# Kernel tuning notes

Measured on AMD Instinct MI355X. Metric: run time of the kernel, lower is better.

Reference implementation:

```python
import jax, jax.numpy as jnp
import numpy as np

N_NODES = 100000
N_EDGES = 1600000
D = 128


def _graph_conv(x, src, dst, norm_src, norm_dst, W, b):
    # DGL GraphConv, norm='both': out = D_dst^{-1/2} A D_src^{-1/2} x W + b
    xs = x * norm_src[:, None]                 # [N, d] scale by src (out-)degree
    agg = jax.ops.segment_sum(xs[src], dst, num_segments=N_NODES)  # SpMM
    hd = agg * norm_dst[:, None]
    return hd @ W + b


def setup_inputs() -> dict:
    key = jax.random.key(0)
    ks = jax.random.split(key, 9)
    h = jax.random.normal(ks[0], (N_NODES, D), dtype=jnp.float32)
    src = jax.random.randint(ks[1], (N_EDGES,), 0, N_NODES, dtype=jnp.int64)
    dst = jax.random.randint(ks[2], (N_EDGES,), 0, N_NODES, dtype=jnp.int64)
    s = 1.0 / np.sqrt(D)
    W0 = jax.random.uniform(ks[3], (D, D), jnp.float32, -s, s)
    b0 = jnp.zeros((D,), jnp.float32)
    W1 = jax.random.uniform(ks[4], (D, D), jnp.float32, -s, s)
    b1 = jnp.zeros((D,), jnp.float32)
    W2 = jax.random.uniform(ks[5], (D, D), jnp.float32, -s, s)
    b2 = jnp.zeros((D,), jnp.float32)
    return {"h": h, "src": src, "dst": dst, "W0": W0, "b0": b0,
            "W1": W1, "b1": b1, "W2": W2, "b2": b2}


def reference(h, src, dst, W0, b0, W1, b1, W2, b2):
    ones = jnp.ones((N_EDGES,), jnp.float32)
    deg_out = jnp.maximum(jax.ops.segment_sum(ones, src, num_segments=N_NODES), 1.0)
    deg_in = jnp.maximum(jax.ops.segment_sum(ones, dst, num_segments=N_NODES), 1.0)
    norm_src = deg_out ** -0.5
    norm_dst = deg_in ** -0.5

    x = jax.nn.relu(_graph_conv(h, src, dst, norm_src, norm_dst, W0, b0))
    x = jax.nn.relu(_graph_conv(x, src, dst, norm_src, norm_dst, W1, b1))
    x = _graph_conv(x, src, dst, norm_src, norm_dst, W2, b2)
    # dgl.mean_nodes over a single graph -> [1, out_size]
    return jnp.mean(x, axis=0, keepdims=True)
```

## Files before the change

kernel.cpp:

```cpp
#include <hip/hip_runtime.h>
#include <hip/hip_fp16.h>

#define N_NODES 100000
#define N_EDGES 1600000
#define D 128
#define SCAN_NB ((N_NODES + 1023) / 1024)
#define CHK 128
#define CHUNK_E (N_EDGES / CHK)
#define HALF_N 50000
#define HALF_U (HALF_N / 4)
#define PP_STRIDE (N_NODES / 4)
#define NSH2 2
#define SH2 (N_NODES / NSH2)
#define SH2_U (SH2 / 4)

typedef _Float16 f16x4 __attribute__((ext_vector_type(4)));
typedef _Float16 f16x8 __attribute__((ext_vector_type(8)));
typedef float f32x4 __attribute__((ext_vector_type(4)));
typedef float f32x2 __attribute__((ext_vector_type(2)));

__global__ __launch_bounds__(256) void
k_zwt(const float* __restrict__ W0, const float* __restrict__ W1,
      __half* __restrict__ Wt, uint4* __restrict__ zbase) {
    if (blockIdx.x < 128) {
        int i = blockIdx.x * 256 + threadIdx.x;
        int l = i >> 14, r = i & (D * D - 1);
        int n = r >> 7, k = r & 127;
        const float* W = l ? W1 : W0;
        Wt[i] = __float2half(W[k * D + n]);
        return;
    }
    int i = (blockIdx.x - 128) * 256 + threadIdx.x;
    if (i < 2 * N_NODES / 4) zbase[i] = (uint4){0u, 0u, 0u, 0u};
}

__global__ __launch_bounds__(256) void
k_hist(const int* __restrict__ src, const int* __restrict__ dst,
       unsigned int* __restrict__ pp, int* __restrict__ cnt_src) {
    __shared__ unsigned int h[HALF_U];
    int b = blockIdx.x;
    int half = b >> 7, c = b & (CHK - 1);
    int lo = half * HALF_N;
    for (int i = threadIdx.x; i < HALF_U; i += 256) h[i] = 0;
    __syncthreads();
    int e0 = c * CHUNK_E;
    int s0 = e0 + half * (CHUNK_E / 2);
    for (int i = s0 + threadIdx.x; i < s0 + CHUNK_E / 2; i += 256)
        atomicAdd(&cnt_src[src[i]], 1);
    for (int i = e0 + threadIdx.x; i < e0 + CHUNK_E; i += 256) {
        int v = dst[i] - lo;
        if ((unsigned)v < HALF_N)
            atomicAdd(&h[v >> 2], 1u << ((v & 3) * 8));
    }
    __syncthreads();
    unsigned int* po = pp + (size_t)c * PP_STRIDE + half * HALF_U;
    for (int i = threadIdx.x; i < HALF_U; i += 256) po[i] = h[i];
}

__global__ void k_merge(unsigned int* __restrict__ pp, int* __restrict__ cnt_dst) {
    int u = blockIdx.x * blockDim.x + threadIdx.x;
    if (u >= PP_STRIDE) return;
    unsigned int* p = pp + u;
    int s0 = 0, s1 = 0, s2 = 0, s3 = 0;
#pragma unroll 8
    for (int c = 0; c < CHK; c++) {
        unsigned int v = p[(size_t)c * PP_STRIDE];
        p[(size_t)c * PP_STRIDE] =
            (unsigned)s0 | ((unsigned)s1 << 8) | ((unsigned)s2 << 16) | ((unsigned)s3 << 24);
        s0 += v & 255; s1 += (v >> 8) & 255; s2 += (v >> 16) & 255; s3 += (v >> 24) & 255;
    }
    cnt_dst[4 * u + 0] = s0; cnt_dst[4 * u + 1] = s1;
    cnt_dst[4 * u + 2] = s2; cnt_dst[4 * u + 3] = s3;
}

__global__ __launch_bounds__(1024) void
k_scan1(const int* __restrict__ cnt_dst, int* __restrict__ rpD,
        int* __restrict__ bsD) {
    __shared__ int s[1024];
    int tid = threadIdx.x;
    int i = blockIdx.x * 1024 + tid;
    int v = (i < N_NODES) ? cnt_dst[i] : 0;
    s[tid] = v;
    __syncthreads();
    for (int d = 1; d < 1024; d <<= 1) {
        int t = (tid >= d) ? s[tid - d] : 0;
        __syncthreads();
        s[tid] += t;
        __syncthreads();
    }
    if (i < N_NODES) rpD[1 + i] = s[tid];
    if (tid == 1023) bsD[blockIdx.x] = s[1023];
}

__global__ void k_scan2(int* __restrict__ bs) {
    __shared__ int s[128];
    int tid = threadIdx.x;
    int v = (tid < SCAN_NB) ? bs[tid] : 0;
    s[tid] = v;
    __syncthreads();
    for (int d = 1; d < 128; d <<= 1) {
        int t = (tid >= d) ? s[tid - d] : 0;
        __syncthreads();
        s[tid] += t;
        __syncthreads();
    }
    if (tid < SCAN_NB) bs[tid] = s[tid] - v;
}

__global__ void k_scan3norm(int* __restrict__ rpD, const int* __restrict__ bsD,
                            const int* __restrict__ cnt_src,
                            const int* __restrict__ cnt_dst,
                            float* __restrict__ ns, float* __restrict__ nd,
                            float* __restrict__ colsum) {
    int i = blockIdx.x * blockDim.x + threadIdx.x;
    if (i >= N_NODES) return;
    rpD[1 + i] += bsD[i >> 10];
    if (i == 0) rpD[0] = 0;
    if (i < 128) colsum[i] = 0.0f;
    ns[i] = rsqrtf((float)max(cnt_src[i], 1));
    nd[i] = rsqrtf((float)max(cnt_dst[i], 1));
}

__global__ __launch_bounds__(256) void
k_scatter(const int* __restrict__ src, const int* __restrict__ dst,
          const int* __restrict__ rpD, const unsigned int* __restrict__ pp,
          const float* __restrict__ nd, int* __restrict__ csr_src,
          float* __restrict__ wsum) {
    __shared__ unsigned int cur[SH2_U];
    int bb = blockIdx.x;
    int sh = bb & 1, c = bb >> 1;
    int lo = sh * SH2;
    for (int i = threadIdx.x; i < SH2_U; i += 256) cur[i] = 0;
    __syncthreads();
    int e0 = c * CHUNK_E;
    const unsigned int* pre = pp + (size_t)c * PP_STRIDE;
    for (int i = e0 + threadIdx.x; i < e0 + CHUNK_E; i += 256) {
        int dfull = dst[i];
        int sfull = src[i];
        int d = dfull - lo;
        if ((unsigned)d < SH2) {
            int sft = (d & 3) * 8;
            int rank = (atomicAdd(&cur[d >> 2], 1u << sft) >> sft) & 255;
            int p8 = (pre[dfull >> 2] >> ((dfull & 3) * 8)) & 255;
            csr_src[rpD[dfull] + p8 + rank] = sfull;
        }
        if ((i & 1) == sh)
            unsafeAtomicAdd(&wsum[sfull], nd[dfull]);
    }
}

__global__ void k_prep(const float* __restrict__ x, const float* __restrict__ ns,
                       unsigned int* __restrict__ out) {
    int i = blockIdx.x * 256 + threadIdx.x;
    if (i >= N_NODES * (D / 4)) return;
    int n = i >> 5;
    float4 v = ((const float4*)x)[i];
    float s = ns[n];
    int u = __builtin_amdgcn_cvt_pk_fp8_f32(v.x * s, v.y * s, 0, false);
    u = __builtin_amdgcn_cvt_pk_fp8_f32(v.z * s, v.w * s, u, true);
    out[i] = (unsigned int)u;
}

__global__ __launch_bounds__(256) void
k_spmm(const unsigned char* __restrict__ x8, const int* __restrict__ row_ptr,
       const int* __restrict__ csr_src, __half* __restrict__ agg) {
    int wave = (blockIdx.x * blockDim.x + threadIdx.x) >> 6;
    int lane = threadIdx.x & 63;
    int hf = lane >> 5, l32 = lane & 31;
    if (wave >= N_NODES) return;
    int beg = row_ptr[wave], end = row_ptr[wave + 1];
    float a0 = 0.f, a1 = 0.f, a2 = 0.f, a3 = 0.f;
    int j = beg;
    for (; j + 7 < end; j += 8) {
#pragma unroll
        for (int p = 0; p < 4; p++) {
            int s0 = csr_src[j + 2 * p];
            int s1 = csr_src[j + 2 * p + 1];
            int s = hf ? s1 : s0;
            unsigned int u = *(const unsigned int*)(x8 + (size_t)s * D + 4 * l32);
            f32x2 lo = __builtin_amdgcn_cvt_pk_f32_fp8(u, false);
            f32x2 hi = __builtin_amdgcn_cvt_pk_f32_fp8(u, true);
            a0 += lo[0]; a1 += lo[1]; a2 += hi[0]; a3 += hi[1];
        }
    }
    for (; j + 1 < end; j += 2) {
        int s0 = csr_src[j], s1 = csr_src[j + 1];
        int s = hf ? s1 : s0;
        unsigned int u = *(const unsigned int*)(x8 + (size_t)s * D + 4 * l32);
        f32x2 lo = __builtin_amdgcn_cvt_pk_f32_fp8(u, false);
        f32x2 hi = __builtin_amdgcn_cvt_pk_f32_fp8(u, true);
        a0 += lo[0]; a1 += lo[1]; a2 += hi[0]; a3 += hi[1];
    }
    if (j < end && hf == 0) {
        int s = csr_src[j];
        unsigned int u = *(const unsigned int*)(x8 + (size_t)s * D + 4 * l32);
        f32x2 lo = __builtin_amdgcn_cvt_pk_f32_fp8(u, false);
        f32x2 hi = __builtin_amdgcn_cvt_pk_f32_fp8(u, true);
        a0 += lo[0]; a1 += lo[1]; a2 += hi[0]; a3 += hi[1];
    }
    a0 += __shfl_xor(a0, 32, 64);
    a1 += __shfl_xor(a1, 32, 64);
    a2 += __shfl_xor(a2, 32, 64);
    a3 += __shfl_xor(a3, 32, 64);
    if (hf == 0) {
        f16x4 o;
        o[0] = (_Float16)a0; o[1] = (_Float16)a1; o[2] = (_Float16)a2; o[3] = (_Float16)a3;
        ((f16x4*)(agg + (size_t)wave * D))[l32] = o;
    }
}

__global__ __launch_bounds__(256) void
k_gemm_mfma(const __half* __restrict__ A, const __half* __restrict__ Wt,
            const float* __restrict__ b, const float* __restrict__ nd,
            const float* __restrict__ ns, unsigned char* __restrict__ out) {
    int w = threadIdx.x >> 6, lane = threadIdx.x & 63;
    int m = lane & 15, q = lane >> 4;
    int row0 = blockIdx.x * 128 + w * 32;

    f16x8 zf;
#pragma unroll
    for (int j = 0; j < 8; j++) zf[j] = (_Float16)0;
    f16x8 af[2][4];
#pragma unroll
    for (int g = 0; g < 2; g++) {
        int arow = row0 + g * 16 + m;
        const f16x8* pa = (const f16x8*)(A + (size_t)arow * D);
        bool aok = arow < N_NODES;
#pragma unroll
        for (int ks = 0; ks < 4; ks++) af[g][ks] = aok ? pa[ks * 4 + q] : zf;
    }

    const f16x8* pb = (const f16x8*)Wt;
    f32x4 acc[2][8];
#pragma unroll
    for (int g = 0; g < 2; g++)
#pragma unroll
        for (int nt = 0; nt < 8; nt++) acc[g][nt] = (f32x4){0.f, 0.f, 0.f, 0.f};

#pragma unroll
    for (int ks = 0; ks < 4; ks++) {
#pragma unroll
        for (int nt = 0; nt < 8; nt++) {
            f16x8 bf = pb[((nt * 16 + m) << 4) + (ks << 2) + q];
            acc[0][nt] = __builtin_amdgcn_mfma_f32_16x16x32_f16(af[0][ks], bf, acc[0][nt], 0, 0, 0);
            acc[1][nt] = __builtin_amdgcn_mfma_f32_16x16x32_f16(af[1][ks], bf, acc[1][nt], 0, 0, 0);
        }
    }

#pragma unroll
    for (int g = 0; g < 2; g++) {
        int er = row0 + g * 16 + q * 4;
        float sd[4], ss[4];
#pragma unroll
        for (int r = 0; r < 4; r++) {
            int n = er + r;
            bool ok = n < N_NODES;
            sd[r] = ok ? nd[n] : 0.0f;
            ss[r] = ok ? ns[n] : 0.0f;
        }
#pragma unroll
        for (int nt = 0; nt < 8; nt++) {
            int col = nt * 16 + m;
            float bc = b[col];
#pragma unroll
            for (int r = 0; r < 4; r++) {
                int n = er + r;
                if (n < N_NODES) {
                    float v = fmaxf(sd[r] * acc[g][nt][r] + bc, 0.0f) * ss[r];
                    int pk = __builtin_amdgcn_cvt_pk_fp8_f32(v, v, 0, false);
                    out[(size_t)n * D + col] = (unsigned char)(pk & 0xff);
                }
            }
        }
    }
}

__global__ __launch_bounds__(256) void
k_gemm_red(const __half* __restrict__ A, const __half* __restrict__ Wt,
           const float* __restrict__ b, const float* __restrict__ nd,
           const float* __restrict__ ns, const float* __restrict__ wsum,
           float* __restrict__ colsum) {
    __shared__ float red[128];
    int tid = threadIdx.x;
    if (tid < 128) red[tid] = 0.0f;
    __syncthreads();

    int w = tid >> 6, lane = tid & 63;
    int m = lane & 15, q = lane >> 4;
    int row0 = blockIdx.x * 128 + w * 32;

    f16x8 zf;
#pragma unroll
    for (int j = 0; j < 8; j++) zf[j] = (_Float16)0;
    f16x8 af[2][4];
#pragma unroll
    for (int g = 0; g < 2; g++) {
        int arow = row0 + g * 16 + m;
        const f16x8* pa = (const f16x8*)(A + (size_t)arow * D);
        bool aok = arow < N_NODES;
#pragma unroll
        for (int ks = 0; ks < 4; ks++) af[g][ks] = aok ? pa[ks * 4 + q] : zf;
    }

    const f16x8* pb = (const f16x8*)Wt;
    f32x4 acc[2][8];
#pragma unroll
    for (int g = 0; g < 2; g++)
#pragma unroll
        for (int nt = 0; nt < 8; nt++) acc[g][nt] = (f32x4){0.f, 0.f, 0.f, 0.f};

#pragma unroll
    for (int ks = 0; ks < 4; ks++) {
#pragma unroll
        for (int nt = 0; nt < 8; nt++) {
            f16x8 bf = pb[((nt * 16 + m) << 4) + (ks << 2) + q];
            acc[0][nt] = __builtin_amdgcn_mfma_f32_16x16x32_f16(af[0][ks], bf, acc[0][nt], 0, 0, 0);
            acc[1][nt] = __builtin_amdgcn_mfma_f32_16x16x32_f16(af[1][ks], bf, acc[1][nt], 0, 0, 0);
        }
    }

    float sd[2][4], sw[2][4];
#pragma unroll
    for (int g = 0; g < 2; g++) {
        int er = row0 + g * 16 + q * 4;
#pragma unroll
        for (int r = 0; r < 4; r++) {
            int n = er + r;
            bool ok = n < N_NODES;
            sd[g][r] = ok ? nd[n] : 0.0f;
            sw[g][r] = ok ? wsum[n] * ns[n] : 0.0f;
        }
    }
#pragma unroll
    for (int nt = 0; nt < 8; nt++) {
        int col = nt * 16 + m;
        float bc = b[col];
        float pc = 0.0f;
#pragma unroll
        for (int g = 0; g < 2; g++)
#pragma unroll
            for (int r = 0; r < 4; r++)
                pc += sw[g][r] * fmaxf(sd[g][r] * acc[g][nt][r] + bc, 0.0f);
        atomicAdd(&red[col], pc);
    }
    __syncthreads();
    if (tid < 128) unsafeAtomicAdd(&colsum[tid], red[tid]);
}

__global__ void k_final(const float* __restrict__ colsum, const float* __restrict__ W,
                        const float* __restrict__ b, float* __restrict__ out) {
    __shared__ float m[128];
    int j = threadIdx.x;
    m[j] = colsum[j] * (1.0f / N_NODES);
    __syncthreads();
    float acc = b[j];
    for (int k = 0; k < 128; k++)
        acc = fmaf(m[k], W[(size_t)k * D + j], acc);
    out[j] = acc;
}

extern "C" void kernel_launch(void* const* d_in, const int* in_sizes, int n_in,
                              void* d_out, int out_size, void* d_ws, size_t ws_size,
                              hipStream_t stream) {
    const float* h   = (const float*)d_in[0];
    const int*   src = (const int*)d_in[1];
    const int*   dst = (const int*)d_in[2];
    const float* W0  = (const float*)d_in[3];
    const float* b0  = (const float*)d_in[4];
    const float* W1  = (const float*)d_in[5];
    const float* b1  = (const float*)d_in[6];
    const float* W2  = (const float*)d_in[7];
    const float* b2  = (const float*)d_in[8];
    float* out = (float*)d_out;

    int*           cnt_src = (int*)d_ws;
    float*         wsum    = (float*)(cnt_src + N_NODES);
    int*           cnt_dst = (int*)(wsum + N_NODES);
    float*         ns      = (float*)(cnt_dst + N_NODES);
    float*         nd      = ns + N_NODES;
    float*         colsum  = nd + N_NODES;
    int*           bsD     = (int*)(colsum + 128);
    int*           rpD     = bsD + 128;
    __half*        Wt16    = (__half*)(rpD + N_NODES + 4);
    int*           csr_src = (int*)(Wt16 + 2 * D * D);
    unsigned int*  pp      = (unsigned int*)(csr_src + N_EDGES);
    unsigned char* x8      = (unsigned char*)pp;
    __half*        agg16   = (__half*)(pp + (size_t)CHK * PP_STRIDE);

    k_zwt<<<128 + (2 * N_NODES / 4 + 255) / 256, 256, 0, stream>>>(
        W0, W1, Wt16, (uint4*)d_ws);
    k_hist<<<2 * CHK, 256, 0, stream>>>(src, dst, pp, cnt_src);
    k_merge<<<(PP_STRIDE + 255) / 256, 256, 0, stream>>>(pp, cnt_dst);
    k_scan1<<<SCAN_NB, 1024, 0, stream>>>(cnt_dst, rpD, bsD);
    k_scan2<<<1, 128, 0, stream>>>(bsD);
    k_scan3norm<<<(N_NODES + 255) / 256, 256, 0, stream>>>(rpD, bsD, cnt_src,
                                                           cnt_dst, ns, nd, colsum);
    k_scatter<<<NSH2 * CHK, 256, 0, stream>>>(src, dst, rpD, pp, nd, csr_src, wsum);

    k_prep<<<(N_NODES * (D / 4) + 255) / 256, 256, 0, stream>>>(h, ns, (unsigned int*)x8);

    k_spmm<<<(N_NODES + 3) / 4, 256, 0, stream>>>(x8, rpD, csr_src, agg16);
    k_gemm_mfma<<<(N_NODES + 127) / 128, 256, 0, stream>>>(agg16, Wt16, b0, nd, ns, x8);
    k_spmm<<<(N_NODES + 3) / 4, 256, 0, stream>>>(x8, rpD, csr_src, agg16);
    k_gemm_red<<<(N_NODES + 127) / 128, 256, 0, stream>>>(agg16, Wt16 + (size_t)D * D,
                                                          b1, nd, ns, wsum, colsum);
    k_final<<<1, 128, 0, stream>>>(colsum, W2, b2, out);
}
```

Before: 500.1 us.

## Split histogram and scatter into eight shards, move src counting into scatter

The dst histogram now runs with eight node-range shards per edge chunk instead of two, and the blocks are indexed so chunks group by XCD. The scatter also uses eight shards and keeps a full-int LDS cursor per node, preloaded with row_ptr plus the per-chunk prefix. This drops the packed-byte rank extraction and the per-edge global reads of rpD and pp. Source-degree counting moves from the histogram into the scatter, and the ns array is removed in favour of computing rsqrt(cnt_src) wherever it is used, which trades more redundant dst/src reads across shards for less LDS contention and fewer global lookups.

```diff
diff --git a/kernel.cpp b/kernel.cpp
--- a/kernel.cpp
+++ b/kernel.cpp
@@ -7,12 +7,12 @@
 #define SCAN_NB ((N_NODES + 1023) / 1024)
 #define CHK 128
 #define CHUNK_E (N_EDGES / CHK)
-#define HALF_N 50000
-#define HALF_U (HALF_N / 4)
 #define PP_STRIDE (N_NODES / 4)
-#define NSH2 2
-#define SH2 (N_NODES / NSH2)
-#define SH2_U (SH2 / 4)
+#define QH 8
+#define QH_N (N_NODES / QH)
+#define QH_U (QH_N / 4)
+#define NSH 8
+#define SH_N (N_NODES / NSH)
 
 typedef _Float16 f16x4 __attribute__((ext_vector_type(4)));
 typedef _Float16 f16x8 __attribute__((ext_vector_type(8)));
@@ -35,26 +35,23 @@
 }
 
 __global__ __launch_bounds__(256) void
-k_hist(const int* __restrict__ src, const int* __restrict__ dst,
-       unsigned int* __restrict__ pp, int* __restrict__ cnt_src) {
-    __shared__ unsigned int h[HALF_U];
+k_hist(const int* __restrict__ dst, unsigned int* __restrict__ pp) {
+    __shared__ unsigned int h[QH_U];
     int b = blockIdx.x;
-    int half = b >> 7, c = b & (CHK - 1);
-    int lo = half * HALF_N;
-    for (int i = threadIdx.x; i < HALF_U; i += 256) h[i] = 0;
+    int xcd = b & 7, slot = b >> 3, g = slot & 7, ci = slot >> 3;
+    int c = xcd * 16 + ci;
+    int lo = g * QH_N;
+    for (int i = threadIdx.x; i < QH_U; i += 256) h[i] = 0;
     __syncthreads();
     int e0 = c * CHUNK_E;
-    int s0 = e0 + half * (CHUNK_E / 2);
-    for (int i = s0 + threadIdx.x; i < s0 + CHUNK_E / 2; i += 256)
-        atomicAdd(&cnt_src[src[i]], 1);
     for (int i = e0 + threadIdx.x; i < e0 + CHUNK_E; i += 256) {
         int v = dst[i] - lo;
-        if ((unsigned)v < HALF_N)
+        if ((unsigned)v < QH_N)
             atomicAdd(&h[v >> 2], 1u << ((v & 3) * 8));
     }
     __syncthreads();
-    unsigned int* po = pp + (size_t)c * PP_STRIDE + half * HALF_U;
-    for (int i = threadIdx.x; i < HALF_U; i += 256) po[i] = h[i];
+    unsigned int* po = pp + (size_t)c * PP_STRIDE + g * QH_U;
+    for (int i = threadIdx.x; i < QH_U; i += 256) po[i] = h[i];
 }
 
 __global__ void k_merge(unsigned int* __restrict__ pp, int* __restrict__ cnt_dst) {
@@ -108,16 +105,13 @@
 }
 
 __global__ void k_scan3norm(int* __restrict__ rpD, const int* __restrict__ bsD,
-                            const int* __restrict__ cnt_src,
                             const int* __restrict__ cnt_dst,
-                            float* __restrict__ ns, float* __restrict__ nd,
-                            float* __restrict__ colsum) {
+                            float* __restrict__ nd, float* __restrict__ colsum) {
     int i = blockIdx.x * blockDim.x + threadIdx.x;
     if (i >= N_NODES) return;
     rpD[1 + i] += bsD[i >> 10];
     if (i == 0) rpD[0] = 0;
     if (i < 128) colsum[i] = 0.0f;
-    ns[i] = rsqrtf((float)max(cnt_src[i], 1));
     nd[i] = rsqrtf((float)max(cnt_dst[i], 1));
 }
 
@@ -125,37 +119,41 @@
 k_scatter(const int* __restrict__ src, const int* __restrict__ dst,
           const int* __restrict__ rpD, const unsigned int* __restrict__ pp,
           const float* __restrict__ nd, int* __restrict__ csr_src,
-          float* __restrict__ wsum) {
-    __shared__ unsigned int cur[SH2_U];
-    int bb = blockIdx.x;
-    int sh = bb & 1, c = bb >> 1;
-    int lo = sh * SH2;
-    for (int i = threadIdx.x; i < SH2_U; i += 256) cur[i] = 0;
+          float* __restrict__ wsum, int* __restrict__ cnt_src) {
+    __shared__ int cur[SH_N];
+    int b = blockIdx.x;
+    int xcd = b & 7, slot = b >> 3, sh = slot & 7, ci = slot >> 3;
+    int c = xcd * 16 + ci;
+    int lo = sh * SH_N;
+    const unsigned int* pre = pp + (size_t)c * PP_STRIDE + (lo >> 2);
+    for (int u = threadIdx.x; u < SH_N; u += 256) {
+        int p8 = (pre[u >> 2] >> ((u & 3) * 8)) & 255;
+        cur[u] = rpD[lo + u] + p8;
+    }
     __syncthreads();
     int e0 = c * CHUNK_E;
-    const unsigned int* pre = pp + (size_t)c * PP_STRIDE;
     for (int i = e0 + threadIdx.x; i < e0 + CHUNK_E; i += 256) {
         int dfull = dst[i];
         int sfull = src[i];
         int d = dfull - lo;
-        if ((unsigned)d < SH2) {
-            int sft = (d & 3) * 8;
-            int rank = (atomicAdd(&cur[d >> 2], 1u << sft) >> sft) & 255;
-            int p8 = (pre[dfull >> 2] >> ((dfull & 3) * 8)) & 255;
-            csr_src[rpD[dfull] + p8 + rank] = sfull;
-        }
-        if ((i & 1) == sh)
+        if ((unsigned)d < SH_N) {
+            int pos = atomicAdd(&cur[d], 1);
+            csr_src[pos] = sfull;
+        }
+        if ((i & 7) == sh) {
             unsafeAtomicAdd(&wsum[sfull], nd[dfull]);
-    }
-}
-
-__global__ void k_prep(const float* __restrict__ x, const float* __restrict__ ns,
+            atomicAdd(&cnt_src[sfull], 1);
+        }
+    }
+}
+
+__global__ void k_prep(const float* __restrict__ x, const int* __restrict__ cnt_src,
                        unsigned int* __restrict__ out) {
     int i = blockIdx.x * 256 + threadIdx.x;
     if (i >= N_NODES * (D / 4)) return;
     int n = i >> 5;
     float4 v = ((const float4*)x)[i];
-    float s = ns[n];
+    float s = rsqrtf((float)max(cnt_src[n], 1));
     int u = __builtin_amdgcn_cvt_pk_fp8_f32(v.x * s, v.y * s, 0, false);
     u = __builtin_amdgcn_cvt_pk_fp8_f32(v.z * s, v.w * s, u, true);
     out[i] = (unsigned int)u;
@@ -212,7 +210,7 @@
 __global__ __launch_bounds__(256) void
 k_gemm_mfma(const __half* __restrict__ A, const __half* __restrict__ Wt,
             const float* __restrict__ b, const float* __restrict__ nd,
-            const float* __restrict__ ns, unsigned char* __restrict__ out) {
+            const int* __restrict__ cnt_src, unsigned char* __restrict__ out) {
     int w = threadIdx.x >> 6, lane = threadIdx.x & 63;
     int m = lane & 15, q = lane >> 4;
     int row0 = blockIdx.x * 128 + w * 32;
@@ -256,7 +254,7 @@
             int n = er + r;
             bool ok = n < N_NODES;
             sd[r] = ok ? nd[n] : 0.0f;
-            ss[r] = ok ? ns[n] : 0.0f;
+            ss[r] = ok ? rsqrtf((float)max(cnt_src[n], 1)) : 0.0f;
         }
 #pragma unroll
         for (int nt = 0; nt < 8; nt++) {
@@ -278,7 +276,7 @@
 __global__ __launch_bounds__(256) void
 k_gemm_red(const __half* __restrict__ A, const __half* __restrict__ Wt,
            const float* __restrict__ b, const float* __restrict__ nd,
-           const float* __restrict__ ns, const float* __restrict__ wsum,
+           const int* __restrict__ cnt_src, const float* __restrict__ wsum,
            float* __restrict__ colsum) {
     __shared__ float red[128];
     int tid = threadIdx.x;
@@ -328,7 +326,7 @@
             int n = er + r;
             bool ok = n < N_NODES;
             sd[g][r] = ok ? nd[n] : 0.0f;
-            sw[g][r] = ok ? wsum[n] * ns[n] : 0.0f;
+            sw[g][r] = ok ? wsum[n] * rsqrtf((float)max(cnt_src[n], 1)) : 0.0f;
         }
     }
 #pragma unroll
@@ -376,8 +374,7 @@
     int*           cnt_src = (int*)d_ws;
     float*         wsum    = (float*)(cnt_src + N_NODES);
     int*           cnt_dst = (int*)(wsum + N_NODES);
-    float*         ns      = (float*)(cnt_dst + N_NODES);
-    float*         nd      = ns + N_NODES;
+    float*         nd      = (float*)(cnt_dst + N_NODES);
     float*         colsum  = nd + N_NODES;
     int*           bsD     = (int*)(colsum + 128);
     int*           rpD     = bsD + 128;
@@ -389,20 +386,23 @@
 
     k_zwt<<<128 + (2 * N_NODES / 4 + 255) / 256, 256, 0, stream>>>(
         W0, W1, Wt16, (uint4*)d_ws);
-    k_hist<<<2 * CHK, 256, 0, stream>>>(src, dst, pp, cnt_src);
+    k_hist<<<QH * CHK, 256, 0, stream>>>(dst, pp);
     k_merge<<<(PP_STRIDE + 255) / 256, 256, 0, stream>>>(pp, cnt_dst);
     k_scan1<<<SCAN_NB, 1024, 0, stream>>>(cnt_dst, rpD, bsD);
     k_scan2<<<1, 128, 0, stream>>>(bsD);
-    k_scan3norm<<<(N_NODES + 255) / 256, 256, 0, stream>>>(rpD, bsD, cnt_src,
-                                                           cnt_dst, ns, nd, colsum);
-    k_scatter<<<NSH2 * CHK, 256, 0, stream>>>(src, dst, rpD, pp, nd, csr_src, wsum);
-
-    k_prep<<<(N_NODES * (D / 4) + 255) / 256, 256, 0, stream>>>(h, ns, (unsigned int*)x8);
+    k_scan3norm<<<(N_NODES + 255) / 256, 256, 0, stream>>>(rpD, bsD, cnt_dst,
+                                                           nd, colsum);
+    k_scatter<<<NSH * CHK, 256, 0, stream>>>(src, dst, rpD, pp, nd,
+                                             csr_src, wsum, cnt_src);
+
+    k_prep<<<(N_NODES * (D / 4) + 255) / 256, 256, 0, stream>>>(h, cnt_src,
+                                                                (unsigned int*)x8);
 
     k_spmm<<<(N_NODES + 3) / 4, 256, 0, stream>>>(x8, rpD, csr_src, agg16);
-    k_gemm_mfma<<<(N_NODES + 127) / 128, 256, 0, stream>>>(agg16, Wt16, b0, nd, ns, x8);
+    k_gemm_mfma<<<(N_NODES + 127) / 128, 256, 0, stream>>>(agg16, Wt16, b0, nd,
+                                                           cnt_src, x8);
     k_spmm<<<(N_NODES + 3) / 4, 256, 0, stream>>>(x8, rpD, csr_src, agg16);
     k_gemm_red<<<(N_NODES + 127) / 128, 256, 0, stream>>>(agg16, Wt16 + (size_t)D * D,
-                                                          b1, nd, ns, wsum, colsum);
+                                                          b1, nd, cnt_src, wsum, colsum);
     k_final<<<1, 128, 0, stream>>>(colsum, W2, b2, out);
 }
```

New measurement: 511.8 us. +2.4%, slower.
